# Kernel tuning notes

Measured on AMD Instinct MI355X. Metric: run time of the kernel, lower is better.

Reference implementation:

```python
import jax, jax.numpy as jnp
import numpy as np

B, H, W, C = 32, 56, 56, 256
NH, WS, SHIFT = 8, 7, 3
S = WS * WS            # tokens per window = 49
CH = C // NH           # channels per head = 32
EPS = 1e-5


def layer_norm(x, w, b):
    mu = jnp.mean(x, axis=-1, keepdims=True)
    var = jnp.var(x, axis=-1, keepdims=True)
    return (x - mu) * jax.lax.rsqrt(var + EPS) * w + b


def spatial_mlp(x, weight, bias):
    # x: (B, H*W, C); weight: (NH*S, S, 1) grouped-conv1d weight; bias: (NH*S,)
    xr = x.reshape(B, H, W, C)
    if SHIFT > 0:
        P_l, P_r, P_t, P_b = WS - SHIFT, SHIFT, WS - SHIFT, SHIFT
        xr = jnp.pad(xr, ((0, 0), (P_t, P_b), (P_l, P_r), (0, 0)))
    Hp, Wp = xr.shape[1], xr.shape[2]
    # window partition -> (nW, S, NH, CH)
    win = xr.reshape(B, Hp // WS, WS, Wp // WS, WS, C)
    win = win.transpose(0, 1, 3, 2, 4, 5).reshape(-1, S, NH, CH)
    # grouped 1x1 conv == per-head token-mixing matrix (S x S)
    wgt = weight.reshape(NH, S, S)             # wgt[h, i, j]
    out = jnp.einsum('hij,njhd->nihd', wgt, win)
    out = out + bias.reshape(NH, S).T[None, :, :, None]
    # window reverse -> (B, Hp, Wp, C)
    out = out.reshape(B, Hp // WS, Wp // WS, WS, WS, C)
    out = out.transpose(0, 1, 3, 2, 4, 5).reshape(B, Hp, Wp, C)
    if SHIFT > 0:
        out = out[:, P_t:Hp - P_b, P_l:Wp - P_r, :]
    return out.reshape(B, H * W, C)


def mlp(x, fc1_w, fc1_b, fc2_w, fc2_b):
    h = jax.nn.gelu(x @ fc1_w + fc1_b, approximate=False)
    return h @ fc2_w + fc2_b


def setup_inputs() -> dict:
    key = jax.random.key(0)
    ks = jax.random.split(key, 5)
    sc = 0.02
    return {
        'x': jax.random.normal(ks[0], (B, H * W, C), jnp.float32),
        'norm1_w': jnp.ones((C,), jnp.float32),
        'norm1_b': jnp.zeros((C,), jnp.float32),
        'spatial_w': jax.random.normal(ks[1], (NH * S, S, 1), jnp.float32) * sc,
        'spatial_b': jax.random.normal(ks[2], (NH * S,), jnp.float32) * sc,
        'norm2_w': jnp.ones((C,), jnp.float32),
        'norm2_b': jnp.zeros((C,), jnp.float32),
        'fc1_w': jax.random.normal(ks[3], (C, 4 * C), jnp.float32) * sc,
        'fc1_b': jnp.zeros((4 * C,), jnp.float32),
        'fc2_w': jax.random.normal(ks[4], (4 * C, C), jnp.float32) * sc,
        'fc2_b': jnp.zeros((C,), jnp.float32),
    }


def reference(x, norm1_w, norm1_b, spatial_w, spatial_b, norm2_w, norm2_b,
              fc1_w, fc1_b, fc2_w, fc2_b):
    shortcut = x
    h = layer_norm(x, norm1_w, norm1_b)
    h = spatial_mlp(h, spatial_w, spatial_b)
    x = shortcut + h                      # drop_path = 0 (eval)
    x = x + mlp(layer_norm(x, norm2_w, norm2_b), fc1_w, fc1_b, fc2_w, fc2_b)
    return x
```

## Files before the change

### kernel.cpp

```cpp
#include <hip/hip_runtime.h>
#include <hip/hip_bf16.h>

#define NHEAD 8
#define IMG   3136
#define MTOT  100352

typedef __attribute__((ext_vector_type(2))) _Float16 f16x2;
typedef __attribute__((ext_vector_type(4))) float    f32x4;
typedef __attribute__((ext_vector_type(16))) float   f32x16;
typedef __attribute__((ext_vector_type(8))) short    bf16x8;
typedef __attribute__((ext_vector_type(2))) int      i32x2;
typedef __attribute__((ext_vector_type(4))) int      i32x4;

#define SWZA(byteoff, r) ((byteoff) ^ (((r)&7)<<4) ^ ((((r)>>3)&1)<<7))

__device__ __forceinline__ short f2bf(float f){
  union { float fv; unsigned u; } a; a.fv = f;
  unsigned u = a.u;
  unsigned r = (u + 0x7fffu + ((u >> 16) & 1u)) >> 16;
  return (short)r;
}

__device__ __forceinline__ unsigned cvtpk(float lo, float hi){
  unsigned r;
  asm("v_cvt_pk_bf16_f32 %0, %1, %2" : "=v"(r) : "v"(lo), "v"(hi));
  return r;
}

__device__ __forceinline__ float gelu_s(float v){
  float e = __expf(-1.702f*v);
  return v*__builtin_amdgcn_rcpf(1.f + e);
}

__global__ void prep_k(const float* __restrict__ fc1w, const float* __restrict__ fc2w,
                       const float* __restrict__ spw,
                       short* __restrict__ w1p, short* __restrict__ w2p,
                       short* __restrict__ wspA)
{
  int bid = blockIdx.x, t = threadIdx.x;
  if (bid < 128) {
    int id = bid*256 + t;
    int l = id & 63, fk = id >> 6;
    int kk = fk & 15, f = fk >> 4;
    int n = f*32 + (l & 31);
    int kbase = kk*16 + (l >> 5)*8;
    bf16x8 o;
    #pragma unroll
    for (int e = 0; e < 8; ++e) o[e] = f2bf(fc1w[(size_t)(kbase+e)*1024 + n]);
    *(bf16x8*)(w1p + (size_t)id*8) = o;
  } else if (bid < 256) {
    int id = (bid-128)*256 + t;
    int l = id & 63, fk = id >> 6;
    int kk = fk & 63, f = fk >> 6;
    int n = f*32 + (l & 31);
    int kbase = kk*16 + (l >> 5)*8;
    bf16x8 o;
    #pragma unroll
    for (int e = 0; e < 8; ++e) o[e] = f2bf(fc2w[(size_t)(kbase+e)*256 + n]);
    *(bf16x8*)(w2p + (size_t)id*8) = o;
  } else {
    #pragma unroll
    for (int k = 0; k < 16; ++k) {
      int idx = t + k*256;
      int lane = idx & 63;
      int kt = (idx >> 6) & 3;
      int mt = (idx >> 8) & 1;
      int h  = idx >> 9;
      int i  = mt*32 + (lane & 31);
      int jb = kt*16 + (lane >> 5)*8;
      bf16x8 o;
      #pragma unroll
      for (int e = 0; e < 8; ++e) {
        int j = jb + e;
        float v = (i < 49 && j < 49) ? spw[(size_t)(h*49 + i)*49 + j] : 0.f;
        o[e] = f2bf(v);
      }
      *(bf16x8*)(wspA + (size_t)idx*8) = o;
    }
  }
}

__global__ __launch_bounds__(512,4) void win_k(
    const float* __restrict__ x, const float* __restrict__ n1w, const float* __restrict__ n1b,
    const float* __restrict__ spb, const short* __restrict__ wspA,
    float* __restrict__ x1)
{
  extern __shared__ char wsm[];
  char*  lxT  = wsm;
  float* murs = (float*)(wsm + 65536);
  int t = threadIdx.x, lane = t & 63, wave = t >> 6;
  int bid = blockIdx.x;

  #pragma unroll
  for (int w = 0; w < 2; ++w) {
    int win = bid*2 + w;
    int b = win/81, rem = win - b*81, wi = rem/9, wj = rem - (rem/9)*9;
    for (int i = wave; i < 49; i += 8) {
      int iy = i/7, ix = i - iy*7;
      int hh = wi*7 + iy - 4, ww = wj*7 + ix - 4;
      if (hh < 0 || hh >= 56 || ww < 0 || ww >= 56) continue;
      const float* row = x + ((size_t)(b*IMG + hh*56 + ww))*256;
      f32x4 v = *(const f32x4*)(row + lane*4);
      float s  = v[0]+v[1]+v[2]+v[3];
      float s2 = v[0]*v[0]+v[1]*v[1]+v[2]*v[2]+v[3]*v[3];
      #pragma unroll
      for (int m = 1; m < 64; m <<= 1) { s += __shfl_xor(s, m); s2 += __shfl_xor(s2, m); }
      float mu = s * (1.f/256.f);
      float rs = rsqrtf(s2*(1.f/256.f) - mu*mu + 1e-5f);
      if (lane == 0) { murs[(w*56+i)*2] = mu; murs[(w*56+i)*2+1] = rs; }
    }
  }
  __syncthreads();

  {
    int w = t >> 8, c = t & 255;
    int win = bid*2 + w;
    int b = win/81, rem = win - b*81, wi = rem/9, wj = rem - (rem/9)*9;
    float nwc = n1w[c], nbc = n1b[c];
    char* rowb = lxT + c*256;
    #pragma unroll
    for (int cj = 0; cj < 7; ++cj) {
      float vals[8];
      #pragma unroll
      for (int e = 0; e < 8; ++e) {
        int p = cj*8 + e;
        float fv = 0.f;
        if (p < 49) {
          int iy = p/7, ix = p - iy*7;
          int hh = wi*7 + iy - 4, ww = wj*7 + ix - 4;
          if (hh >= 0 && hh < 56 && ww >= 0 && ww < 56) {
            float mu = murs[(w*56+p)*2], rs = murs[(w*56+p)*2+1];
            float xv = x[((size_t)(b*IMG + hh*56 + ww))*256 + c];
            fv = (xv - mu)*rs*nwc + nbc;
          }
        }
        vals[e] = fv;
      }
      i32x4 pk;
      pk[0] = cvtpk(vals[0], vals[1]); pk[1] = cvtpk(vals[2], vals[3]);
      pk[2] = cvtpk(vals[4], vals[5]); pk[3] = cvtpk(vals[6], vals[7]);
      *(i32x4*)(rowb + SWZA(w*128 + cj*16, c)) = pk;
    }
    i32x4 z = {0,0,0,0};
    *(i32x4*)(rowb + SWZA(w*128 + 112, c)) = z;
  }
  __syncthreads();

  int h = wave, d = lane & 31, lk = lane >> 5;
  const short* wA = wspA + h*4096;
  int c = h*32 + d;
  f32x16 a00, a01, a10, a11;
  #pragma unroll
  for (int q = 0; q < 16; ++q) { a00[q]=0.f; a01[q]=0.f; a10[q]=0.f; a11[q]=0.f; }
  #pragma unroll
  for (int kt = 0; kt < 4; ++kt) {
    bf16x8 A0 = *(const bf16x8*)(wA + (kt*64 + lane)*8);
    bf16x8 A1 = *(const bf16x8*)(wA + ((4+kt)*64 + lane)*8);
    int bo = kt*32 + lk*16;
    bf16x8 B0 = *(const bf16x8*)(lxT + c*256 + SWZA(bo, c));
    bf16x8 B1 = *(const bf16x8*)(lxT + c*256 + SWZA(128 + bo, c));
    a00 = __builtin_amdgcn_mfma_f32_32x32x16_bf16(A0, B0, a00, 0,0,0);
    a10 = __builtin_amdgcn_mfma_f32_32x32x16_bf16(A1, B0, a10, 0,0,0);
    a01 = __builtin_amdgcn_mfma_f32_32x32x16_bf16(A0, B1, a01, 0,0,0);
    a11 = __builtin_amdgcn_mfma_f32_32x32x16_bf16(A1, B1, a11, 0,0,0);
  }

  #pragma unroll
  for (int w = 0; w < 2; ++w) {
    int win = bid*2 + w;
    int b = win/81, rem = win - b*81, wi = rem/9, wj = rem - (rem/9)*9;
    #pragma unroll
    for (int mt = 0; mt < 2; ++mt) {
      #pragma unroll
      for (int r = 0; r < 16; ++r) {
        int i = mt*32 + (r&3) + 8*(r>>2) + 4*lk;
        if (i < 49) {
          int iy = i/7, ix = i - iy*7;
          int hh = wi*7 + iy - 4, ww = wj*7 + ix - 4;
          if (hh >= 0 && hh < 56 && ww >= 0 && ww < 56) {
            size_t off = ((size_t)(b*IMG + hh*56 + ww))*256 + c;
            float av = mt==0 ? (w==0 ? a00[r] : a01[r]) : (w==0 ? a10[r] : a11[r]);
            x1[off] = x[off] + av + spb[h*49 + i];
          }
        }
      }
    }
  }
}

__global__ __launch_bounds__(512,4) void mlp_k(
    const float* __restrict__ x1, float* __restrict__ out,
    const short* __restrict__ w1p, const short* __restrict__ w2p,
    const float* __restrict__ n2w, const float* __restrict__ n2b,
    const float* __restrict__ b1, const float* __restrict__ b2)
{
  extern __shared__ char sm[];
  char* a2  = sm;
  char* hcb = sm + 32768;

  int t = threadIdx.x, lane = t & 63, wave = t >> 6;
  int m0 = blockIdx.x * 64;

  {
    f32x4 nw = *(const f32x4*)(n2w + lane*4);
    f32x4 nb = *(const f32x4*)(n2b + lane*4);
    #pragma unroll
    for (int rq = 0; rq < 8; ++rq) {
      int rr = wave*8 + rq;
      f32x4 v = *(const f32x4*)(x1 + (size_t)(m0+rr)*256 + lane*4);
      float s  = v[0]+v[1]+v[2]+v[3];
      float s2 = v[0]*v[0]+v[1]*v[1]+v[2]*v[2]+v[3]*v[3];
      #pragma unroll
      for (int m = 1; m < 64; m <<= 1){ s += __shfl_xor(s,m); s2 += __shfl_xor(s2,m); }
      float mu = s*(1.f/256.f);
      float rs = rsqrtf(s2*(1.f/256.f) - mu*mu + 1e-5f);
      float y0 = (v[0]-mu)*rs*nw[0] + nb[0];
      float y1 = (v[1]-mu)*rs*nw[1] + nb[1];
      float y2 = (v[2]-mu)*rs*nw[2] + nb[2];
      float y3 = (v[3]-mu)*rs*nw[3] + nb[3];
      i32x2 pk; pk[0] = cvtpk(y0,y1); pk[1] = cvtpk(y2,y3);
      *(i32x2*)(a2 + SWZA(lane*8, rr) + rr*512) = pk;
    }
  }
  __syncthreads();

  int lr = lane & 31, lk = lane >> 5;
  int wn = wave;

  f32x16 accO[2];
  #pragma unroll
  for (int i=0;i<2;++i)
    #pragma unroll
    for (int q=0;q<16;++q) accO[i][q] = 0.f;

  for (int ch = 0; ch < 4; ++ch) {
    f32x16 accH[2];
    #pragma unroll
    for (int i=0;i<2;++i)
      #pragma unroll
      for (int q=0;q<16;++q) accH[i][q] = 0.f;

    const short* w1f = w1p + ((size_t)((ch*8 + wn)*16)*64 + lane)*8;
    bf16x8 bq[4];
    #pragma unroll
    for (int k = 0; k < 4; ++k) bq[k] = *(const bf16x8*)(w1f + (size_t)k*512);
    __builtin_amdgcn_s_setprio(1);
    #pragma unroll
    for (int kk = 0; kk < 16; ++kk) {
      bf16x8 b = bq[kk & 3];
      if (kk < 12) bq[kk & 3] = *(const bf16x8*)(w1f + (size_t)(kk+4)*512);
      int kb = kk*32 + lk*16;
      bf16x8 a0 = *(const bf16x8*)(a2 + SWZA(kb, lr) + lr*512);
      bf16x8 a1 = *(const bf16x8*)(a2 + SWZA(kb, 32+lr) + (32+lr)*512);
      accH[0] = __builtin_amdgcn_mfma_f32_32x32x16_bf16(a0, b, accH[0], 0,0,0);
      accH[1] = __builtin_amdgcn_mfma_f32_32x32x16_bf16(a1, b, accH[1], 0,0,0);
    }
    __builtin_amdgcn_s_setprio(0);

    {
      float b1v = b1[ch*256 + wn*32 + lr];
      int colb = (wn*32 + lr)*2;
      #pragma unroll
      for (int ms = 0; ms < 2; ++ms) {
        #pragma unroll
        for (int r2 = 0; r2 < 8; ++r2) {
          int r = r2*2;
          float g0 = gelu_s(accH[ms][r]   + b1v);
          float g1 = gelu_s(accH[ms][r+1] + b1v);
          unsigned pw = cvtpk(g0, g1);
          int row0 = ms*32 + (r&3) + 8*(r>>2) + 4*lk;
          int row1 = row0 + 1;
          *(short*)(hcb + SWZA(colb, row0) + row0*512) = (short)(pw & 0xffffu);
          *(short*)(hcb + SWZA(colb, row1) + row1*512) = (short)(pw >> 16);
        }
      }
    }
    __syncthreads();

    const short* w2f = w2p + ((size_t)(wn*64 + ch*16)*64 + lane)*8;
    #pragma unroll
    for (int k = 0; k < 4; ++k) bq[k] = *(const bf16x8*)(w2f + (size_t)k*512);
    __builtin_amdgcn_s_setprio(1);
    #pragma unroll
    for (int kk = 0; kk < 16; ++kk) {
      bf16x8 b = bq[kk & 3];
      if (kk < 12) bq[kk & 3] = *(const bf16x8*)(w2f + (size_t)(kk+4)*512);
      int kb = kk*32 + lk*16;
      bf16x8 a0 = *(const bf16x8*)(hcb + SWZA(kb, lr) + lr*512);
      bf16x8 a1 = *(const bf16x8*)(hcb + SWZA(kb, 32+lr) + (32+lr)*512);
      accO[0] = __builtin_amdgcn_mfma_f32_32x32x16_bf16(a0, b, accO[0], 0,0,0);
      accO[1] = __builtin_amdgcn_mfma_f32_32x32x16_bf16(a1, b, accO[1], 0,0,0);
    }
    __builtin_amdgcn_s_setprio(0);
    __syncthreads();
  }

  {
    int col = wn*32 + lr;
    float b2v = b2[col];
    #pragma unroll
    for (int ms = 0; ms < 2; ++ms) {
      #pragma unroll
      for (int r = 0; r < 16; ++r) {
        int row = ms*32 + (r&3) + 8*(r>>2) + 4*lk;
        size_t off = (size_t)(m0 + row)*256 + col;
        out[off] = x1[off] + accO[ms][r] + b2v;
      }
    }
  }
}

extern "C" void kernel_launch(void* const* d_in, const int* in_sizes, int n_in,
                              void* d_out, int out_size, void* d_ws, size_t ws_size,
                              hipStream_t stream) {
  const float* x    = (const float*)d_in[0];
  const float* n1w  = (const float*)d_in[1];
  const float* n1b  = (const float*)d_in[2];
  const float* spw  = (const float*)d_in[3];
  const float* spb  = (const float*)d_in[4];
  const float* n2w  = (const float*)d_in[5];
  const float* n2b  = (const float*)d_in[6];
  const float* fc1w = (const float*)d_in[7];
  const float* fc1b = (const float*)d_in[8];
  const float* fc2w = (const float*)d_in[9];
  const float* fc2b = (const float*)d_in[10];
  float* outp = (float*)d_out;

  char* ws = (char*)d_ws;
  short* w1p  = (short*)ws;
  short* w2p  = (short*)(ws + 524288);
  short* wspA = (short*)(ws + 1048576);

  prep_k<<<257, 256, 0, stream>>>(fc1w, fc2w, spw, w1p, w2p, wspA);

  hipFuncSetAttribute(reinterpret_cast<const void*>(win_k),
                      hipFuncAttributeMaxDynamicSharedMemorySize, 66432);
  win_k<<<1296, 512, 66432, stream>>>(x, n1w, n1b, spb, wspA, outp);

  hipFuncSetAttribute(reinterpret_cast<const void*>(mlp_k),
                      hipFuncAttributeMaxDynamicSharedMemorySize, 65536);
  mlp_k<<<MTOT/64, 512, 65536, stream>>>(outp, outp, w1p, w2p, n2w, n2b, fc1b, fc2b);
}
```

Before: 290.3 us.

## Shrink MLP tile to 32 rows with double-buffered hidden chunks

Restructures the fused LayerNorm+MLP kernel to process 32 rows per block with 4 waves instead of 64 rows with 8 waves. The hidden dimension is now walked in 128-wide chunks with two ping-pong LDS buffers, which removes the trailing barrier per chunk. Each wave now owns 64 output columns in the second GEMM, and the first fc1 weight loads are prefetched before the LayerNorm phase. LDS per block halves and the block count doubles, which should raise occupancy and overlap. In exchange, each weight fragment is reused across half as many rows, so L2 weight traffic per output row rises.

```diff
diff --git a/kernel.cpp b/kernel.cpp
--- a/kernel.cpp
+++ b/kernel.cpp
@@ -13,6 +13,7 @@
 typedef __attribute__((ext_vector_type(4))) int      i32x4;
 
 #define SWZA(byteoff, r) ((byteoff) ^ (((r)&7)<<4) ^ ((((r)>>3)&1)<<7))
+#define SWZC(byteoff, r) ((byteoff) ^ (((r)&7)<<4) ^ ((((r)>>3)&1)<<7))
 
 __device__ __forceinline__ short f2bf(float f){
   union { float fv; unsigned u; } a; a.fv = f;
@@ -188,7 +189,7 @@
   }
 }
 
-__global__ __launch_bounds__(512,4) void mlp_k(
+__global__ __launch_bounds__(256,4) void mlp_k(
     const float* __restrict__ x1, float* __restrict__ out,
     const short* __restrict__ w1p, const short* __restrict__ w2p,
     const float* __restrict__ n2w, const float* __restrict__ n2b,
@@ -196,10 +197,20 @@
 {
   extern __shared__ char sm[];
   char* a2  = sm;
-  char* hcb = sm + 32768;
+  char* hc0 = sm + 16384;
+  char* hc1 = sm + 24576;
 
   int t = threadIdx.x, lane = t & 63, wave = t >> 6;
-  int m0 = blockIdx.x * 64;
+  int m0 = blockIdx.x * 32;
+  int lr = lane & 31, lk = lane >> 5;
+  int wn = wave;
+
+  const short* g1 = w1p + ((size_t)(wn*16)*64 + lane)*8;
+  const short* g2 = w2p + ((size_t)((wn*2)*64)*64 + lane)*8;
+
+  bf16x8 bq[4];
+  #pragma unroll
+  for (int k = 0; k < 4; ++k) bq[k] = *(const bf16x8*)(g1 + (size_t)k*512);
 
   {
     f32x4 nw = *(const f32x4*)(n2w + lane*4);
@@ -224,88 +235,87 @@
   }
   __syncthreads();
 
-  int lr = lane & 31, lk = lane >> 5;
-  int wn = wave;
-
   f32x16 accO[2];
   #pragma unroll
   for (int i=0;i<2;++i)
     #pragma unroll
     for (int q=0;q<16;++q) accO[i][q] = 0.f;
 
-  for (int ch = 0; ch < 4; ++ch) {
-    f32x16 accH[2];
-    #pragma unroll
-    for (int i=0;i<2;++i)
-      #pragma unroll
-      for (int q=0;q<16;++q) accH[i][q] = 0.f;
-
-    const short* w1f = w1p + ((size_t)((ch*8 + wn)*16)*64 + lane)*8;
-    bf16x8 bq[4];
-    #pragma unroll
-    for (int k = 0; k < 4; ++k) bq[k] = *(const bf16x8*)(w1f + (size_t)k*512);
+  for (int ch = 0; ch < 8; ++ch) {
+    f32x16 accH;
+    #pragma unroll
+    for (int q=0;q<16;++q) accH[q] = 0.f;
+
     __builtin_amdgcn_s_setprio(1);
     #pragma unroll
     for (int kk = 0; kk < 16; ++kk) {
       bf16x8 b = bq[kk & 3];
-      if (kk < 12) bq[kk & 3] = *(const bf16x8*)(w1f + (size_t)(kk+4)*512);
+      if (kk < 12) bq[kk & 3] = *(const bf16x8*)(g1 + (size_t)(kk+4)*512);
       int kb = kk*32 + lk*16;
       bf16x8 a0 = *(const bf16x8*)(a2 + SWZA(kb, lr) + lr*512);
-      bf16x8 a1 = *(const bf16x8*)(a2 + SWZA(kb, 32+lr) + (32+lr)*512);
-      accH[0] = __builtin_amdgcn_mfma_f32_32x32x16_bf16(a0, b, accH[0], 0,0,0);
-      accH[1] = __builtin_amdgcn_mfma_f32_32x32x16_bf16(a1, b, accH[1], 0,0,0);
+      accH = __builtin_amdgcn_mfma_f32_32x32x16_bf16(a0, b, accH, 0,0,0);
     }
     __builtin_amdgcn_s_setprio(0);
 
+    bq[0] = *(const bf16x8*)(g2 + (size_t)0*512);
+    bq[1] = *(const bf16x8*)(g2 + (size_t)64*512);
+    bq[2] = *(const bf16x8*)(g2 + (size_t)1*512);
+    bq[3] = *(const bf16x8*)(g2 + (size_t)65*512);
+
+    char* hcw = (ch & 1) ? hc1 : hc0;
+
     {
-      float b1v = b1[ch*256 + wn*32 + lr];
+      float b1v = b1[ch*128 + wn*32 + lr];
       int colb = (wn*32 + lr)*2;
       #pragma unroll
-      for (int ms = 0; ms < 2; ++ms) {
-        #pragma unroll
-        for (int r2 = 0; r2 < 8; ++r2) {
-          int r = r2*2;
-          float g0 = gelu_s(accH[ms][r]   + b1v);
-          float g1 = gelu_s(accH[ms][r+1] + b1v);
-          unsigned pw = cvtpk(g0, g1);
-          int row0 = ms*32 + (r&3) + 8*(r>>2) + 4*lk;
-          int row1 = row0 + 1;
-          *(short*)(hcb + SWZA(colb, row0) + row0*512) = (short)(pw & 0xffffu);
-          *(short*)(hcb + SWZA(colb, row1) + row1*512) = (short)(pw >> 16);
-        }
+      for (int r2 = 0; r2 < 8; ++r2) {
+        int r = r2*2;
+        float g0 = gelu_s(accH[r]   + b1v);
+        float g1v = gelu_s(accH[r+1] + b1v);
+        unsigned pw = cvtpk(g0, g1v);
+        int row0 = (r&3) + 8*(r>>2) + 4*lk;
+        int row1 = row0 + 1;
+        *(short*)(hcw + SWZC(colb, row0) + row0*256) = (short)(pw & 0xffffu);
+        *(short*)(hcw + SWZC(colb, row1) + row1*256) = (short)(pw >> 16);
       }
     }
     __syncthreads();
 
-    const short* w2f = w2p + ((size_t)(wn*64 + ch*16)*64 + lane)*8;
-    #pragma unroll
-    for (int k = 0; k < 4; ++k) bq[k] = *(const bf16x8*)(w2f + (size_t)k*512);
     __builtin_amdgcn_s_setprio(1);
     #pragma unroll
-    for (int kk = 0; kk < 16; ++kk) {
-      bf16x8 b = bq[kk & 3];
-      if (kk < 12) bq[kk & 3] = *(const bf16x8*)(w2f + (size_t)(kk+4)*512);
+    for (int kk = 0; kk < 8; ++kk) {
+      bf16x8 b0, b1f;
+      if ((kk&1)==0) { b0 = bq[0]; b1f = bq[1]; } else { b0 = bq[2]; b1f = bq[3]; }
+      if (kk < 6) {
+        bf16x8 n0 = *(const bf16x8*)(g2 + (size_t)(kk+2)*512);
+        bf16x8 n1 = *(const bf16x8*)(g2 + (size_t)(64+kk+2)*512);
+        if ((kk&1)==0) { bq[0] = n0; bq[1] = n1; } else { bq[2] = n0; bq[3] = n1; }
+      }
       int kb = kk*32 + lk*16;
-      bf16x8 a0 = *(const bf16x8*)(hcb + SWZA(kb, lr) + lr*512);
-      bf16x8 a1 = *(const bf16x8*)(hcb + SWZA(kb, 32+lr) + (32+lr)*512);
-      accO[0] = __builtin_amdgcn_mfma_f32_32x32x16_bf16(a0, b, accO[0], 0,0,0);
-      accO[1] = __builtin_amdgcn_mfma_f32_32x32x16_bf16(a1, b, accO[1], 0,0,0);
+      bf16x8 a0 = *(const bf16x8*)(hcw + SWZC(kb, lr) + lr*256);
+      accO[0] = __builtin_amdgcn_mfma_f32_32x32x16_bf16(a0, b0, accO[0], 0,0,0);
+      accO[1] = __builtin_amdgcn_mfma_f32_32x32x16_bf16(a0, b1f, accO[1], 0,0,0);
     }
     __builtin_amdgcn_s_setprio(0);
-    __syncthreads();
-  }
-
-  {
-    int col = wn*32 + lr;
+
+    g1 += (size_t)64*512;
+    g2 += (size_t)8*512;
+    if (ch < 7) {
+      #pragma unroll
+      for (int k = 0; k < 4; ++k) bq[k] = *(const bf16x8*)(g1 + (size_t)k*512);
+    }
+  }
+
+  #pragma unroll
+  for (int ns = 0; ns < 2; ++ns) {
+    int col = wn*64 + ns*32 + lr;
     float b2v = b2[col];
     #pragma unroll
-    for (int ms = 0; ms < 2; ++ms) {
-      #pragma unroll
-      for (int r = 0; r < 16; ++r) {
-        int row = ms*32 + (r&3) + 8*(r>>2) + 4*lk;
-        size_t off = (size_t)(m0 + row)*256 + col;
-        out[off] = x1[off] + accO[ms][r] + b2v;
-      }
+    for (int r = 0; r < 16; ++r) {
+      int row = (r&3) + 8*(r>>2) + 4*lk;
+      size_t off = (size_t)(m0 + row)*256 + col;
+      float av = ns==0 ? accO[0][r] : accO[1][r];
+      out[off] = x1[off] + av + b2v;
     }
   }
 }
@@ -338,6 +348,6 @@
   win_k<<<1296, 512, 66432, stream>>>(x, n1w, n1b, spb, wspA, outp);
 
   hipFuncSetAttribute(reinterpret_cast<const void*>(mlp_k),
-                      hipFuncAttributeMaxDynamicSharedMemorySize, 65536);
-  mlp_k<<<MTOT/64, 512, 65536, stream>>>(outp, outp, w1p, w2p, n2w, n2b, fc1b, fc2b);
-}
+                      hipFuncAttributeMaxDynamicSharedMemorySize, 32768);
+  mlp_k<<<MTOT/32, 256, 32768, stream>>>(outp, outp, w1p, w2p, n2w, n2b, fc1b, fc2b);
+}
```

New measurement: 302.5 us. +4.2%, slower.
